# Kernel tuning notes

Measured on AMD Instinct MI355X. Metric: run time of the kernel, lower is better.

## Reference

```python
import jax, jax.numpy as jnp
import numpy as np

N_HEADS = 16
EPS = 1e-5
ROPE_BASE = 10000.0


def setup_inputs() -> dict:
    key = jax.random.key(0)
    ks = jax.random.split(key, 5)
    B, T, C = 2, 2048, 2048
    s = 0.02
    return {
        "x": jax.random.normal(ks[0], (B, T, C), dtype=jnp.float32),
        "rms_weight": jnp.ones((C,), dtype=jnp.float32),
        "qkv_w": jax.random.normal(ks[1], (3 * C, C), dtype=jnp.float32) * s,
        "qkv_b": jax.random.normal(ks[2], (3 * C,), dtype=jnp.float32) * s,
        "o_w": jax.random.normal(ks[3], (C, C), dtype=jnp.float32) * s,
        "o_b": jax.random.normal(ks[4], (C,), dtype=jnp.float32) * s,
    }


def _rotate_half(t):
    half = t.shape[-1] // 2
    return jnp.concatenate([-t[..., half:], t[..., :half]], axis=-1)


def reference(x, rms_weight, qkv_w, qkv_b, o_w, o_b):
    B, T, C = x.shape
    H = N_HEADS
    D = C // H

    # RMSNorm
    xn = x * jax.lax.rsqrt(jnp.mean(x * x, axis=-1, keepdims=True) + EPS) * rms_weight

    # fused QKV projection -> [B, T, 3, H, D]
    qkv = (xn @ qkv_w.T + qkv_b).reshape(B, T, 3, H, D)
    q, k, v = qkv[:, :, 0], qkv[:, :, 1], qkv[:, :, 2]

    # RoPE (position_ids = arange(T))
    pos = jnp.arange(T, dtype=jnp.float32)
    inv_freq = 1.0 / (ROPE_BASE ** (jnp.arange(0, D, 2, dtype=jnp.float32) / D))
    freqs = pos[:, None] * inv_freq[None, :]          # [T, D/2]
    emb = jnp.concatenate([freqs, freqs], axis=-1)     # [T, D]
    cos = jnp.cos(emb)[None, :, None, :]               # [1, T, 1, D]
    sin = jnp.sin(emb)[None, :, None, :]
    q = q * cos + _rotate_half(q) * sin
    k = k * cos + _rotate_half(k) * sin

    # causal attention (flash_attn_func semantics, dropout=0)
    scale = 1.0 / jnp.sqrt(jnp.asarray(D, dtype=x.dtype))
    scores = jnp.einsum("bqhd,bkhd->bhqk", q, k) * scale
    causal = jnp.tril(jnp.ones((T, T), dtype=bool))
    scores = jnp.where(causal[None, None], scores, jnp.asarray(-1e30, scores.dtype))
    attn = jax.nn.softmax(scores, axis=-1)
    out = jnp.einsum("bhqk,bkhd->bqhd", attn, v).reshape(B, T, C)

    # output projection
    return out @ o_w.T + o_b
```

## Files before the change

kernel.cpp:

```cpp
#include <hip/hip_runtime.h>
#include <stdint.h>

typedef __attribute__((ext_vector_type(8))) short bf16x8;
typedef __attribute__((ext_vector_type(4))) float f32x4;

typedef __attribute__((address_space(3))) uint32_t lds_u32_t;
typedef __attribute__((address_space(1))) const uint32_t glb_u32_t;

static __device__ __forceinline__ ushort f2bf(float f) {
  uint32_t u = __float_as_uint(f);
  uint32_t r = (u + 0x7FFFu + ((u >> 16) & 1u)) >> 16;
  return (ushort)r;
}
static __device__ __forceinline__ float bf2f(ushort u) {
  return __uint_as_float(((uint32_t)u) << 16);
}
static __device__ __forceinline__ ushort cvt1(float f) {
  uint32_t u;
  asm("v_cvt_pk_bf16_f32 %0, %1, %1" : "=v"(u) : "v"(f));
  return (ushort)u;
}
static __device__ __forceinline__ float exp2f_fast(float x) {
  float r;
  asm("v_exp_f32 %0, %1" : "=v"(r) : "v"(x));
  return r;
}

__global__ __launch_bounds__(256) void prologue_kernel(
    const float* __restrict__ x, const float* __restrict__ rmsw,
    ushort* __restrict__ xn, const float* __restrict__ qkv_w,
    ushort* __restrict__ wq, const float* __restrict__ o_w,
    ushort* __restrict__ wo, float* __restrict__ cs, float* __restrict__ sn) {
  const int C = 2048;
  int blk = blockIdx.x;
  int tid = threadIdx.x;
  if (blk < 4096) {
    int lane = tid & 63, wid = tid >> 6;
    const float* xr = x + (size_t)blk * C;
    float4 a = ((const float4*)xr)[tid * 2];
    float4 b = ((const float4*)xr)[tid * 2 + 1];
    float ss = a.x * a.x + a.y * a.y + a.z * a.z + a.w * a.w +
               b.x * b.x + b.y * b.y + b.z * b.z + b.w * b.w;
#pragma unroll
    for (int off = 1; off < 64; off <<= 1) ss += __shfl_xor(ss, off);
    __shared__ float part[4];
    if (lane == 0) part[wid] = ss;
    __syncthreads();
    float tot = part[0] + part[1] + part[2] + part[3];
    float inv = rsqrtf(tot * (1.0f / 2048.0f) + 1e-5f);
    float4 wa = ((const float4*)rmsw)[tid * 2];
    float4 wb = ((const float4*)rmsw)[tid * 2 + 1];
    ushort* dst = xn + (size_t)blk * C + tid * 8;
    ushort4 o0, o1;
    o0.x = f2bf(a.x * inv * wa.x); o0.y = f2bf(a.y * inv * wa.y);
    o0.z = f2bf(a.z * inv * wa.z); o0.w = f2bf(a.w * inv * wa.w);
    o1.x = f2bf(b.x * inv * wb.x); o1.y = f2bf(b.y * inv * wb.y);
    o1.z = f2bf(b.z * inv * wb.z); o1.w = f2bf(b.w * inv * wb.w);
    ((ushort4*)dst)[0] = o0;
    ((ushort4*)dst)[1] = o1;
  } else if (blk < 4096 + 512) {
    int idx = (blk - 4096) * 256 + tid;
    int t = idx >> 6, j = idx & 63;
    float inv_freq = expf(-(2.0f * (float)j / 128.0f) * 9.210340371976184f);
    float ang = (float)t * inv_freq;
    cs[idx] = cosf(ang);
    sn[idx] = sinf(ang);
  } else {
    const int n1 = 6144 * 2048 / 4, n2 = 2048 * 2048 / 4;
    int stride = 1280 * 256;
    for (int i = (blk - 4608) * 256 + tid; i < n1 + n2; i += stride) {
      const float* src = (i < n1) ? qkv_w : o_w;
      ushort* dst = (i < n1) ? wq : wo;
      int k = (i < n1) ? i : i - n1;
      float4 v = ((const float4*)src)[k];
      ushort4 o;
      o.x = f2bf(v.x); o.y = f2bf(v.y); o.z = f2bf(v.z); o.w = f2bf(v.w);
      ((ushort4*)dst)[k] = o;
    }
  }
}

template <int EPI>
__global__ __launch_bounds__(512, 2) void gemm3p_kernel(
    const ushort* __restrict__ A, const ushort* __restrict__ W,
    const float* __restrict__ bias, ushort* __restrict__ qb,
    ushort* __restrict__ kb, ushort* __restrict__ vb, float* __restrict__ out,
    const float* __restrict__ cs, const float* __restrict__ sn) {
  const int K = 2048;
  __shared__ ushort lA[3][128 * 64];
  __shared__ ushort lB[3][256 * 64];
  const int tid = threadIdx.x;
  const int lane = tid & 63;
  const int wid = tid >> 6;
  const int wr = wid >> 2;
  const int wc = wid & 3;
  const int ar = lane & 15, g = lane >> 4;

  int cpx = gridDim.x >> 3;
  int swzb = ((int)blockIdx.x & 7) * cpx + ((int)blockIdx.x >> 3);
  int tm = swzb & 31, tn = swzb >> 5;
  int row0 = tm * 128, col0 = tn * 256;

  auto stageA = [&](int slot, int kt) {
#pragma unroll
    for (int i = 0; i < 2; ++i) {
      int e = (i * 512 + tid) * 16;
      int r = e >> 7, b = e & 127;
      int sb = b ^ ((r & 7) << 4);
      __builtin_amdgcn_global_load_lds(
          (glb_u32_t*)(A + (size_t)(row0 + r) * K + kt * 64 + (sb >> 1)),
          (lds_u32_t*)((char*)lA[slot] + e), 16, 0, 0);
    }
  };
  auto stageB1 = [&](int slot, int kt, int i) {
    int e = (i * 512 + tid) * 16;
    int r = e >> 7, b = e & 127;
    int sb = b ^ ((r & 7) << 4);
    __builtin_amdgcn_global_load_lds(
        (glb_u32_t*)(W + (size_t)(col0 + r) * K + kt * 64 + (sb >> 1)),
        (lds_u32_t*)((char*)lB[slot] + e), 16, 0, 0);
  };

  f32x4 acc[4][4];
#pragma unroll
  for (int m = 0; m < 4; ++m)
#pragma unroll
    for (int n = 0; n < 4; ++n) acc[m][n] = (f32x4){0.f, 0.f, 0.f, 0.f};

  stageA(0, 0);
#pragma unroll
  for (int i = 0; i < 4; ++i) stageB1(0, 0, i);
  stageA(1, 1);
#pragma unroll
  for (int i = 0; i < 4; ++i) stageB1(1, 1, i);
  asm volatile("s_waitcnt vmcnt(6)" ::: "memory");
  asm volatile("s_barrier" ::: "memory");

  const int NT = K / 64;
  int cur = 0;
  for (int kt = 0; kt < NT; ++kt) {
    int s2 = cur + 2; if (s2 >= 3) s2 -= 3;
    const char* lAp = (const char*)lA[cur];
    const char* lBp = (const char*)lB[cur];
    const bool pf = (kt + 2 < NT);
    bf16x8 bF[4][2], aF[2][2];
#pragma unroll
    for (int n = 0; n < 4; ++n) {
      int rr = (wc + n * 4) * 16 + ar;
      int sw = (rr & 7) << 4;
#pragma unroll
      for (int ks = 0; ks < 2; ++ks)
        bF[n][ks] = *(const bf16x8*)(lBp + rr * 128 + ((ks * 64 + g * 16) ^ sw));
    }
#pragma unroll
    for (int m = 0; m < 2; ++m) {
      int rr = wr * 64 + m * 16 + ar;
      int sw = (rr & 7) << 4;
#pragma unroll
      for (int ks = 0; ks < 2; ++ks)
        aF[m][ks] = *(const bf16x8*)(lAp + rr * 128 + ((ks * 64 + g * 16) ^ sw));
    }
    if (pf) { stageA(s2, kt + 2); stageB1(s2, kt + 2, 0); }
    asm volatile("s_barrier" ::: "memory");
    __builtin_amdgcn_s_setprio(1);
#pragma unroll
    for (int m = 0; m < 2; ++m)
#pragma unroll
      for (int n = 0; n < 4; ++n)
#pragma unroll
        for (int ks = 0; ks < 2; ++ks)
          acc[m][n] = __builtin_amdgcn_mfma_f32_16x16x32_bf16(aF[m][ks], bF[n][ks],
                                                              acc[m][n], 0, 0, 0);
    __builtin_amdgcn_s_setprio(0);
    bf16x8 aG[2][2];
#pragma unroll
    for (int m = 0; m < 2; ++m) {
      int rr = wr * 64 + (2 + m) * 16 + ar;
      int sw = (rr & 7) << 4;
#pragma unroll
      for (int ks = 0; ks < 2; ++ks)
        aG[m][ks] = *(const bf16x8*)(lAp + rr * 128 + ((ks * 64 + g * 16) ^ sw));
    }
    if (pf) { stageB1(s2, kt + 2, 1); stageB1(s2, kt + 2, 2); stageB1(s2, kt + 2, 3); }
    if (kt < NT - 2) {
      asm volatile("s_waitcnt vmcnt(6)" ::: "memory");
    } else if (kt == NT - 2) {
      asm volatile("s_waitcnt vmcnt(0)" ::: "memory");
    }
    asm volatile("s_barrier" ::: "memory");
    __builtin_amdgcn_s_setprio(1);
#pragma unroll
    for (int m = 0; m < 2; ++m)
#pragma unroll
      for (int n = 0; n < 4; ++n)
#pragma unroll
        for (int ks = 0; ks < 2; ++ks)
          acc[2 + m][n] = __builtin_amdgcn_mfma_f32_16x16x32_bf16(aG[m][ks], bF[n][ks],
                                                                  acc[2 + m][n], 0, 0, 0);
    __builtin_amdgcn_s_setprio(0);
    cur = cur + 1; if (cur >= 3) cur = 0;
  }

  if constexpr (EPI == 0) {
    int s = col0 >> 11;
    int dlo = wc * 16 + ar;
    int hbase = (col0 >> 7) & 15;
    float bv[4];
#pragma unroll
    for (int n = 0; n < 4; ++n) bv[n] = bias[col0 + dlo + n * 64];
    if (s < 2) {
      ushort* dst = (s == 0) ? qb : kb;
      const float oscale = (s == 0) ? 0.12751551132892735f : 1.0f;
      const float* csj = cs + dlo;
      const float* snj = sn + dlo;
#pragma unroll
      for (int m = 0; m < 4; ++m) {
#pragma unroll
        for (int r = 0; r < 4; ++r) {
          int mrow = row0 + wr * 64 + m * 16 + g * 4 + r;
          int bb = mrow >> 11, t = mrow & 2047;
          float cc = csj[t * 64], sv = snj[t * 64];
          size_t rowbase = ((size_t)(bb * 16 + hbase) * 2048 + t) * 128;
          float lo = acc[m][0][r] + bv[0], hi = acc[m][1][r] + bv[1];
          dst[rowbase + dlo] = cvt1((lo * cc - hi * sv) * oscale);
          dst[rowbase + dlo + 64] = cvt1((hi * cc + lo * sv) * oscale);
          size_t rowbase1 = rowbase + (size_t)2048 * 128;
          lo = acc[m][2][r] + bv[2]; hi = acc[m][3][r] + bv[3];
          dst[rowbase1 + dlo] = cvt1((lo * cc - hi * sv) * oscale);
          dst[rowbase1 + dlo + 64] = cvt1((hi * cc + lo * sv) * oscale);
        }
      }
    } else {
#pragma unroll
      for (int n = 0; n < 4; ++n) {
        int d = dlo + (n & 1) * 64;
        int hh = hbase + (n >> 1);
        float bvn = bv[n];
#pragma unroll
        for (int m = 0; m < 4; ++m) {
          int t0 = row0 + wr * 64 + m * 16 + g * 4;
          int bb = t0 >> 11, tt0 = t0 & 2047;
          ushort4 o;
          o.x = f2bf(acc[m][n][0] + bvn);
          o.y = f2bf(acc[m][n][1] + bvn);
          o.z = f2bf(acc[m][n][2] + bvn);
          o.w = f2bf(acc[m][n][3] + bvn);
          *(ushort4*)&vb[(((size_t)(bb * 16 + hh) * 128) + d) * 2048 + tt0] = o;
        }
      }
    }
  } else {
#pragma unroll
    for (int n = 0; n < 4; ++n) {
      int col = col0 + wc * 16 + ar + n * 64;
      float bvn = bias[col];
#pragma unroll
      for (int m = 0; m < 4; ++m) {
#pragma unroll
        for (int r = 0; r < 4; ++r) {
          int mrow = row0 + wr * 64 + m * 16 + g * 4 + r;
          out[(size_t)mrow * 2048 + col] = acc[m][n][r] + bvn;
        }
      }
    }
  }
}

__global__ __launch_bounds__(512, 4) void attn_kernel(const ushort* __restrict__ Q,
                                                      const ushort* __restrict__ K,
                                                      const ushort* __restrict__ Vt,
                                                      ushort* __restrict__ O) {
  __shared__ ushort kT[2][64 * 128];
  __shared__ ushort vT[2][128 * 64];
  __shared__ ushort plds[8][16][64];
  const int tid = threadIdx.x;
  const int lane = tid & 63, wid = tid >> 6;
  const int ar = lane & 15, g = lane >> 4;
  int blk = blockIdx.x;
  int xcd = blk & 7, jj = blk >> 3;
  int bh = xcd * 4 + (jj >> 4);
  int qq = jj & 15;
  int qt = (jj < 32) ? (15 - qq) : qq;
  int b = bh >> 4, h = bh & 15;
  const ushort* Qb = Q + (size_t)bh * (2048 * 128);
  const ushort* Kb = K + (size_t)bh * (2048 * 128);
  const ushort* Vtb = Vt + (size_t)bh * (128 * 2048);
  int qrow0 = qt * 128 + wid * 16;

  auto stage = [&](int buf, int tt) {
    int kv0 = tt * 64;
#pragma unroll
    for (int i = 0; i < 2; ++i) {
      int e = (i * 512 + tid) * 16;
      {
        int r = e >> 8, bs = (e & 255) ^ ((r & 7) << 4);
        __builtin_amdgcn_global_load_lds(
            (glb_u32_t*)(Kb + (size_t)(kv0 + r) * 128 + (bs >> 1)),
            (lds_u32_t*)((char*)kT[buf] + e), 16, 0, 0);
      }
      {
        int r = e >> 7, bs = (e & 127) ^ ((r & 7) << 4);
        __builtin_amdgcn_global_load_lds(
            (glb_u32_t*)(Vtb + (size_t)r * 2048 + kv0 + (bs >> 1)),
            (lds_u32_t*)((char*)vT[buf] + e), 16, 0, 0);
      }
    }
  };

  bf16x8 qf[4];
#pragma unroll
  for (int kk = 0; kk < 4; ++kk)
    qf[kk] = *(const bf16x8*)&Qb[(size_t)(qrow0 + ar) * 128 + kk * 32 + g * 8];
  bf16x8 vone;
#pragma unroll
  for (int jv = 0; jv < 8; ++jv) vone[jv] = (short)0x3F80;
  float m_r[4] = {-1e30f, -1e30f, -1e30f, -1e30f};
  f32x4 lacc = (f32x4){0.f, 0.f, 0.f, 0.f};
  f32x4 accO[8];
#pragma unroll
  for (int n = 0; n < 8; ++n) accO[n] = (f32x4){0.f, 0.f, 0.f, 0.f};

  int nt = 2 * qt + 2;
  stage(0, 0);
  __syncthreads();
  for (int tt = 0; tt < nt; ++tt) {
    int cb = tt & 1;
    if (tt + 1 < nt) stage(cb ^ 1, tt + 1);
    int kv0 = tt * 64;
    if (kv0 <= qrow0 + 15) {
      const ushort* kTb = kT[cb];
      const ushort* vTb = vT[cb];
      f32x4 s4[4];
      __builtin_amdgcn_s_setprio(1);
#pragma unroll
      for (int n = 0; n < 4; ++n) {
        s4[n] = (f32x4){0.f, 0.f, 0.f, 0.f};
        int r = n * 16 + ar;
        int swz = (r & 7) << 4;
#pragma unroll
        for (int kk = 0; kk < 4; ++kk) {
          int byte = (kk * 64 + g * 16) ^ swz;
          bf16x8 kf = *(const bf16x8*)&kTb[((r << 8) + byte) >> 1];
          s4[n] = __builtin_amdgcn_mfma_f32_16x16x32_bf16(qf[kk], kf, s4[n], 0, 0, 0);
        }
      }
      __builtin_amdgcn_s_setprio(0);
      const bool masked = (kv0 + 63 > qrow0);
      float pv[4][4];
      float pmax[4];
#pragma unroll
      for (int r = 0; r < 4; ++r) {
        float v0 = s4[0][r], v1 = s4[1][r], v2 = s4[2][r], v3 = s4[3][r];
        if (masked) {
          int row = qrow0 + g * 4 + r;
          v0 = (kv0 + ar > row) ? -1e30f : v0;
          v1 = (kv0 + 16 + ar > row) ? -1e30f : v1;
          v2 = (kv0 + 32 + ar > row) ? -1e30f : v2;
          v3 = (kv0 + 48 + ar > row) ? -1e30f : v3;
        }
        float mx = fmaxf(fmaxf(v0, v1), fmaxf(v2, v3));
#pragma unroll
        for (int off = 1; off < 16; off <<= 1) mx = fmaxf(mx, __shfl_xor(mx, off));
        pmax[r] = mx;
        pv[r][0] = v0; pv[r][1] = v1; pv[r][2] = v2; pv[r][3] = v3;
      }
      int nore = (pmax[0] - m_r[0] <= 8.f) && (pmax[1] - m_r[1] <= 8.f) &&
                 (pmax[2] - m_r[2] <= 8.f) && (pmax[3] - m_r[3] <= 8.f);
      if (!__all(nore)) {
#pragma unroll
        for (int r = 0; r < 4; ++r) {
          float mn = fmaxf(m_r[r], pmax[r]);
          float c = exp2f_fast(m_r[r] - mn);
          m_r[r] = mn;
          lacc[r] *= c;
#pragma unroll
          for (int n = 0; n < 8; ++n) accO[n][r] *= c;
        }
      }
#pragma unroll
      for (int r = 0; r < 4; ++r) {
        int qr = g * 4 + r;
        int key = ((qr & 7) << 4) ^ ((qr & 8) << 2);
        char* prow = (char*)&plds[wid][0][0] + qr * 128;
#pragma unroll
        for (int n = 0; n < 4; ++n) {
          float p = exp2f_fast(pv[r][n] - m_r[r]);
          *(ushort*)(prow + ((32 * n + 2 * ar) ^ key)) = cvt1(p);
        }
      }
      asm volatile("s_waitcnt lgkmcnt(0)" ::: "memory");
      int keyr = ((ar & 7) << 4) ^ ((ar & 8) << 2);
      const char* pbase = (const char*)&plds[wid][0][0] + ar * 128;
      bf16x8 pf0 = *(const bf16x8*)(pbase + ((g * 16) ^ keyr));
      bf16x8 pf1 = *(const bf16x8*)(pbase + ((64 + g * 16) ^ keyr));
      __builtin_amdgcn_s_setprio(1);
#pragma unroll
      for (int n = 0; n < 8; ++n) {
        int r = n * 16 + ar;
        int swz = (r & 7) << 4;
        bf16x8 vf0 = *(const bf16x8*)&vTb[((r << 7) + ((g * 16) ^ swz)) >> 1];
        accO[n] = __builtin_amdgcn_mfma_f32_16x16x32_bf16(pf0, vf0, accO[n], 0, 0, 0);
        bf16x8 vf1 = *(const bf16x8*)&vTb[((r << 7) + ((64 + g * 16) ^ swz)) >> 1];
        accO[n] = __builtin_amdgcn_mfma_f32_16x16x32_bf16(pf1, vf1, accO[n], 0, 0, 0);
      }
      lacc = __builtin_amdgcn_mfma_f32_16x16x32_bf16(pf0, vone, lacc, 0, 0, 0);
      lacc = __builtin_amdgcn_mfma_f32_16x16x32_bf16(pf1, vone, lacc, 0, 0, 0);
      __builtin_amdgcn_s_setprio(0);
    }
    __syncthreads();
  }
#pragma unroll
  for (int r = 0; r < 4; ++r) {
    int trow = qrow0 + g * 4 + r;
    float invl = 1.0f / lacc[r];
    ushort* orow = O + ((size_t)b * 2048 + trow) * 2048 + h * 128;
#pragma unroll
    for (int n = 0; n < 8; ++n) orow[n * 16 + ar] = cvt1(accO[n][r] * invl);
  }
}

extern "C" void kernel_launch(void* const* d_in, const int* in_sizes, int n_in,
                              void* d_out, int out_size, void* d_ws, size_t ws_size,
                              hipStream_t stream) {
  const float* x = (const float*)d_in[0];
  const float* rmsw = (const float*)d_in[1];
  const float* qkv_w = (const float*)d_in[2];
  const float* qkv_b = (const float*)d_in[3];
  const float* o_w = (const float*)d_in[4];
  const float* o_b = (const float*)d_in[5];
  float* out = (float*)d_out;

  char* ws = (char*)d_ws;
  size_t off = 0;
  auto alloc = [&](size_t bytes) {
    void* p = ws + off;
    off += (bytes + 255) & ~(size_t)255;
    return p;
  };
  ushort* xn = (ushort*)alloc((size_t)4096 * 2048 * 2);
  ushort* wq = (ushort*)alloc((size_t)6144 * 2048 * 2);
  ushort* wo = (ushort*)alloc((size_t)2048 * 2048 * 2);
  ushort* qb = (ushort*)alloc((size_t)32 * 2048 * 128 * 2);
  ushort* kb = (ushort*)alloc((size_t)32 * 2048 * 128 * 2);
  ushort* vb = (ushort*)alloc((size_t)32 * 2048 * 128 * 2);
  float* cs = (float*)alloc((size_t)2048 * 64 * 4);
  float* sn = (float*)alloc((size_t)2048 * 64 * 4);

  prologue_kernel<<<5888, 256, 0, stream>>>(x, rmsw, xn, qkv_w, wq, o_w, wo, cs, sn);
  gemm3p_kernel<0><<<768, 512, 0, stream>>>(xn, wq, qkv_b, qb, kb, vb, nullptr, cs, sn);
  attn_kernel<<<512, 512, 0, stream>>>(qb, kb, vb, xn );
  gemm3p_kernel<1><<<256, 512, 0, stream>>>(xn, wo, o_b, nullptr, nullptr, nullptr, out,
                                            nullptr, nullptr);
}
```

Measured before the change: 274.5 us.

## Use 256x256 double-buffered tile GEMM for QKV projection

Adds a dedicated QKV GEMM kernel with 256x256 output tiles (each wave computing 128x64) and two LDS buffers instead of the 128x256 triple-buffered kernel, halving the grid to 384 blocks. Larger tiles raise arithmetic intensity and cut redundant global loads of A and W, at the cost of more accumulator registers, more LDS, and a full vmcnt(0) wait every k-step. It also removes one s_barrier in the output-projection GEMM loop and specializes that kernel to the plain epilogue. Dropping the barrier may open a race on the triple-buffered LDS slots.

```diff
diff --git a/kernel.cpp b/kernel.cpp
--- a/kernel.cpp
+++ b/kernel.cpp
@@ -80,12 +80,169 @@
   }
 }
 
-template <int EPI>
+__global__ __launch_bounds__(512, 2) void gemm256_kernel(
+    const ushort* __restrict__ A, const ushort* __restrict__ W,
+    const float* __restrict__ bias, ushort* __restrict__ qb,
+    ushort* __restrict__ kb, ushort* __restrict__ vb,
+    const float* __restrict__ cs, const float* __restrict__ sn) {
+  const int K = 2048;
+  __shared__ ushort lA[2][256 * 64];
+  __shared__ ushort lB[2][256 * 64];
+  const int tid = threadIdx.x;
+  const int lane = tid & 63;
+  const int wid = tid >> 6;
+  const int wr = wid >> 2;
+  const int wc = wid & 3;
+  const int ar = lane & 15, g = lane >> 4;
+
+  int cpx = gridDim.x >> 3;
+  int swzb = ((int)blockIdx.x & 7) * cpx + ((int)blockIdx.x >> 3);
+  int tm = swzb & 15, tn = swzb >> 4;
+  int row0 = tm * 256, col0 = tn * 256;
+
+  auto stageA = [&](int slot, int kt) {
+#pragma unroll
+    for (int i = 0; i < 4; ++i) {
+      int e = (i * 512 + tid) * 16;
+      int r = e >> 7, b = e & 127;
+      int sb = b ^ ((r & 7) << 4);
+      __builtin_amdgcn_global_load_lds(
+          (glb_u32_t*)(A + (size_t)(row0 + r) * K + kt * 64 + (sb >> 1)),
+          (lds_u32_t*)((char*)lA[slot] + e), 16, 0, 0);
+    }
+  };
+  auto stageB = [&](int slot, int kt) {
+#pragma unroll
+    for (int i = 0; i < 4; ++i) {
+      int e = (i * 512 + tid) * 16;
+      int r = e >> 7, b = e & 127;
+      int sb = b ^ ((r & 7) << 4);
+      __builtin_amdgcn_global_load_lds(
+          (glb_u32_t*)(W + (size_t)(col0 + r) * K + kt * 64 + (sb >> 1)),
+          (lds_u32_t*)((char*)lB[slot] + e), 16, 0, 0);
+    }
+  };
+
+  f32x4 acc[8][4];
+#pragma unroll
+  for (int m = 0; m < 8; ++m)
+#pragma unroll
+    for (int n = 0; n < 4; ++n) acc[m][n] = (f32x4){0.f, 0.f, 0.f, 0.f};
+
+  stageA(0, 0);
+  stageB(0, 0);
+  asm volatile("s_waitcnt vmcnt(0)" ::: "memory");
+  asm volatile("s_barrier" ::: "memory");
+
+  const int NT = K / 64;
+  for (int kt = 0; kt < NT; ++kt) {
+    int cb = kt & 1, nb = cb ^ 1;
+    const char* lAp = (const char*)lA[cb];
+    const char* lBp = (const char*)lB[cb];
+    const bool pf = (kt + 1 < NT);
+    bf16x8 bF[4][2], aF[4][2];
+#pragma unroll
+    for (int n = 0; n < 4; ++n) {
+      int rr = (wc + n * 4) * 16 + ar;
+      int sw = (rr & 7) << 4;
+#pragma unroll
+      for (int ks = 0; ks < 2; ++ks)
+        bF[n][ks] = *(const bf16x8*)(lBp + rr * 128 + ((ks * 64 + g * 16) ^ sw));
+    }
+#pragma unroll
+    for (int m = 0; m < 4; ++m) {
+      int rr = wr * 128 + m * 16 + ar;
+      int sw = (rr & 7) << 4;
+#pragma unroll
+      for (int ks = 0; ks < 2; ++ks)
+        aF[m][ks] = *(const bf16x8*)(lAp + rr * 128 + ((ks * 64 + g * 16) ^ sw));
+    }
+    if (pf) { stageA(nb, kt + 1); stageB(nb, kt + 1); }
+    __builtin_amdgcn_s_setprio(1);
+#pragma unroll
+    for (int m = 0; m < 4; ++m)
+#pragma unroll
+      for (int n = 0; n < 4; ++n)
+#pragma unroll
+        for (int ks = 0; ks < 2; ++ks)
+          acc[m][n] = __builtin_amdgcn_mfma_f32_16x16x32_bf16(aF[m][ks], bF[n][ks],
+                                                              acc[m][n], 0, 0, 0);
+    __builtin_amdgcn_s_setprio(0);
+    bf16x8 aG[4][2];
+#pragma unroll
+    for (int m = 0; m < 4; ++m) {
+      int rr = wr * 128 + (4 + m) * 16 + ar;
+      int sw = (rr & 7) << 4;
+#pragma unroll
+      for (int ks = 0; ks < 2; ++ks)
+        aG[m][ks] = *(const bf16x8*)(lAp + rr * 128 + ((ks * 64 + g * 16) ^ sw));
+    }
+    asm volatile("s_waitcnt vmcnt(0)" ::: "memory");
+    asm volatile("s_barrier" ::: "memory");
+    __builtin_amdgcn_s_setprio(1);
+#pragma unroll
+    for (int m = 0; m < 4; ++m)
+#pragma unroll
+      for (int n = 0; n < 4; ++n)
+#pragma unroll
+        for (int ks = 0; ks < 2; ++ks)
+          acc[4 + m][n] = __builtin_amdgcn_mfma_f32_16x16x32_bf16(aG[m][ks], bF[n][ks],
+                                                                  acc[4 + m][n], 0, 0, 0);
+    __builtin_amdgcn_s_setprio(0);
+  }
+
+  int s = col0 >> 11;
+  int dlo = wc * 16 + ar;
+  int hbase = (col0 >> 7) & 15;
+  float bv[4];
+#pragma unroll
+  for (int n = 0; n < 4; ++n) bv[n] = bias[col0 + dlo + n * 64];
+  if (s < 2) {
+    ushort* dst = (s == 0) ? qb : kb;
+    const float oscale = (s == 0) ? 0.12751551132892735f : 1.0f;
+    const float* csj = cs + dlo;
+    const float* snj = sn + dlo;
+#pragma unroll
+    for (int m = 0; m < 8; ++m) {
+#pragma unroll
+      for (int r = 0; r < 4; ++r) {
+        int mrow = row0 + wr * 128 + m * 16 + g * 4 + r;
+        int bb = mrow >> 11, t = mrow & 2047;
+        float cc = csj[t * 64], sv = snj[t * 64];
+        size_t rowbase = ((size_t)(bb * 16 + hbase) * 2048 + t) * 128;
+        float lo = acc[m][0][r] + bv[0], hi = acc[m][1][r] + bv[1];
+        dst[rowbase + dlo] = cvt1((lo * cc - hi * sv) * oscale);
+        dst[rowbase + dlo + 64] = cvt1((hi * cc + lo * sv) * oscale);
+        size_t rowbase1 = rowbase + (size_t)2048 * 128;
+        lo = acc[m][2][r] + bv[2]; hi = acc[m][3][r] + bv[3];
+        dst[rowbase1 + dlo] = cvt1((lo * cc - hi * sv) * oscale);
+        dst[rowbase1 + dlo + 64] = cvt1((hi * cc + lo * sv) * oscale);
+      }
+    }
+  } else {
+#pragma unroll
+    for (int n = 0; n < 4; ++n) {
+      int d = dlo + (n & 1) * 64;
+      int hh = hbase + (n >> 1);
+      float bvn = bv[n];
+#pragma unroll
+      for (int m = 0; m < 8; ++m) {
+        int t0 = row0 + wr * 128 + m * 16 + g * 4;
+        int bb = t0 >> 11, tt0 = t0 & 2047;
+        ushort4 o;
+        o.x = f2bf(acc[m][n][0] + bvn);
+        o.y = f2bf(acc[m][n][1] + bvn);
+        o.z = f2bf(acc[m][n][2] + bvn);
+        o.w = f2bf(acc[m][n][3] + bvn);
+        *(ushort4*)&vb[(((size_t)(bb * 16 + hh) * 128) + d) * 2048 + tt0] = o;
+      }
+    }
+  }
+}
+
 __global__ __launch_bounds__(512, 2) void gemm3p_kernel(
     const ushort* __restrict__ A, const ushort* __restrict__ W,
-    const float* __restrict__ bias, ushort* __restrict__ qb,
-    ushort* __restrict__ kb, ushort* __restrict__ vb, float* __restrict__ out,
-    const float* __restrict__ cs, const float* __restrict__ sn) {
+    const float* __restrict__ bias, float* __restrict__ out) {
   const int K = 2048;
   __shared__ ushort lA[3][128 * 64];
   __shared__ ushort lB[3][256 * 64];
@@ -161,7 +318,6 @@
         aF[m][ks] = *(const bf16x8*)(lAp + rr * 128 + ((ks * 64 + g * 16) ^ sw));
     }
     if (pf) { stageA(s2, kt + 2); stageB1(s2, kt + 2, 0); }
-    asm volatile("s_barrier" ::: "memory");
     __builtin_amdgcn_s_setprio(1);
 #pragma unroll
     for (int m = 0; m < 2; ++m)
@@ -201,66 +357,16 @@
     cur = cur + 1; if (cur >= 3) cur = 0;
   }
 
-  if constexpr (EPI == 0) {
-    int s = col0 >> 11;
-    int dlo = wc * 16 + ar;
-    int hbase = (col0 >> 7) & 15;
-    float bv[4];
-#pragma unroll
-    for (int n = 0; n < 4; ++n) bv[n] = bias[col0 + dlo + n * 64];
-    if (s < 2) {
-      ushort* dst = (s == 0) ? qb : kb;
-      const float oscale = (s == 0) ? 0.12751551132892735f : 1.0f;
-      const float* csj = cs + dlo;
-      const float* snj = sn + dlo;
-#pragma unroll
-      for (int m = 0; m < 4; ++m) {
-#pragma unroll
-        for (int r = 0; r < 4; ++r) {
-          int mrow = row0 + wr * 64 + m * 16 + g * 4 + r;
-          int bb = mrow >> 11, t = mrow & 2047;
-          float cc = csj[t * 64], sv = snj[t * 64];
-          size_t rowbase = ((size_t)(bb * 16 + hbase) * 2048 + t) * 128;
-          float lo = acc[m][0][r] + bv[0], hi = acc[m][1][r] + bv[1];
-          dst[rowbase + dlo] = cvt1((lo * cc - hi * sv) * oscale);
-          dst[rowbase + dlo + 64] = cvt1((hi * cc + lo * sv) * oscale);
-          size_t rowbase1 = rowbase + (size_t)2048 * 128;
-          lo = acc[m][2][r] + bv[2]; hi = acc[m][3][r] + bv[3];
-          dst[rowbase1 + dlo] = cvt1((lo * cc - hi * sv) * oscale);
-          dst[rowbase1 + dlo + 64] = cvt1((hi * cc + lo * sv) * oscale);
-        }
-      }
-    } else {
-#pragma unroll
-      for (int n = 0; n < 4; ++n) {
-        int d = dlo + (n & 1) * 64;
-        int hh = hbase + (n >> 1);
-        float bvn = bv[n];
-#pragma unroll
-        for (int m = 0; m < 4; ++m) {
-          int t0 = row0 + wr * 64 + m * 16 + g * 4;
-          int bb = t0 >> 11, tt0 = t0 & 2047;
-          ushort4 o;
-          o.x = f2bf(acc[m][n][0] + bvn);
-          o.y = f2bf(acc[m][n][1] + bvn);
-          o.z = f2bf(acc[m][n][2] + bvn);
-          o.w = f2bf(acc[m][n][3] + bvn);
-          *(ushort4*)&vb[(((size_t)(bb * 16 + hh) * 128) + d) * 2048 + tt0] = o;
-        }
-      }
-    }
-  } else {
-#pragma unroll
-    for (int n = 0; n < 4; ++n) {
-      int col = col0 + wc * 16 + ar + n * 64;
-      float bvn = bias[col];
-#pragma unroll
-      for (int m = 0; m < 4; ++m) {
-#pragma unroll
-        for (int r = 0; r < 4; ++r) {
-          int mrow = row0 + wr * 64 + m * 16 + g * 4 + r;
-          out[(size_t)mrow * 2048 + col] = acc[m][n][r] + bvn;
-        }
+#pragma unroll
+  for (int n = 0; n < 4; ++n) {
+    int col = col0 + wc * 16 + ar + n * 64;
+    float bvn = bias[col];
+#pragma unroll
+    for (int m = 0; m < 4; ++m) {
+#pragma unroll
+      for (int r = 0; r < 4; ++r) {
+        int mrow = row0 + wr * 64 + m * 16 + g * 4 + r;
+        out[(size_t)mrow * 2048 + col] = acc[m][n][r] + bvn;
       }
     }
   }
@@ -447,8 +553,7 @@
   float* sn = (float*)alloc((size_t)2048 * 64 * 4);
 
   prologue_kernel<<<5888, 256, 0, stream>>>(x, rmsw, xn, qkv_w, wq, o_w, wo, cs, sn);
-  gemm3p_kernel<0><<<768, 512, 0, stream>>>(xn, wq, qkv_b, qb, kb, vb, nullptr, cs, sn);
+  gemm256_kernel<<<384, 512, 0, stream>>>(xn, wq, qkv_b, qb, kb, vb, cs, sn);
   attn_kernel<<<512, 512, 0, stream>>>(qb, kb, vb, xn );
-  gemm3p_kernel<1><<<256, 512, 0, stream>>>(xn, wo, o_b, nullptr, nullptr, nullptr, out,
-                                            nullptr, nullptr);
-}
+  gemm3p_kernel<<<256, 512, 0, stream>>>(xn, wo, o_b, out);
+}
```

New measurement: 277.7 us. Within noise of the previous version (+1.1%).
